# Optimization experiments

Hardware: AMD Instinct MI355X
Metric: run time of the kernel (lower is better)

## Reference

```python
import jax, jax.numpy as jnp
import numpy as np

# config
BSZ, L_, DM = 4, 2048, 1024
H, G, P, N, R = 16, 4, 64, 64, 2
RATIO = H // G            # 4
E, K = 64, 2              # kmoe experts / top_k
DPROJ = H * P * 2 + G * N * R * 2 + G * 3  # 3084


def rms(x, w, eps=1e-5):
    return x * jax.lax.rsqrt(jnp.mean(x * x, axis=-1, keepdims=True) + eps) * w


def kron_moe(x, router_w, A_e, B_e, scale, bias, d1, d2, o1, o2, k):
    # x: [..., d1*d2] -> [..., o1*o2]
    orig = x.shape
    xf = x.reshape(-1, d1 * d2)
    logits = xf @ router_w.T                       # [T, E]
    vals, idx = jax.lax.top_k(logits, k)           # [T, k]
    probs = jax.nn.softmax(vals, axis=-1)
    xs = xf.reshape(-1, d1, d2)
    # Y[t,k,o,p] = sum_ij A[t,k,o,i] x[t,i,j] B[t,k,p,j]
    Y = jnp.einsum('tkoi,tij,tkpj->tkop', A_e[idx], xs, B_e[idx])
    out = jnp.sum(Y * probs[:, :, None, None], axis=1).reshape(orig[:-1] + (o1 * o2,))
    return out * scale + bias


def setup_inputs() -> dict:
    key = jax.random.key(0)
    ks = jax.random.split(key, 12)
    r = lambda k, s, sc: jax.random.normal(k, s, jnp.float32) * sc
    return dict(
        u=jax.random.normal(ks[0], (BSZ, L_, DM), jnp.float32),
        in_proj_w=r(ks[1], (DPROJ, DM), 0.02),
        in_proj_b=jnp.zeros((DPROJ,), jnp.float32),
        xup_router=r(ks[2], (E, P), 0.02),
        xup_A=r(ks[3], (E, 8, 8), 0.1),
        xup_B=r(ks[4], (E, 16, 8), 0.1),
        xup_scale=jnp.ones((1,), jnp.float32),
        xup_bias=jnp.zeros((P * R,), jnp.float32),
        ydown_w=r(ks[5], (P, P * R), 0.02),
        oup_router=r(ks[6], (E, H * P), 0.02),
        oup_A=r(ks[7], (E, 32, 32), 0.05),
        oup_B=r(ks[8], (E, 32, 32), 0.05),
        oup_scale=jnp.ones((1,), jnp.float32),
        oup_bias=jnp.zeros((DM,), jnp.float32),
        theta_log=r(ks[9], (G, N // 2), 1.0),
        D=jnp.ones((H,), jnp.float32),
        normB_w=jnp.ones((N * R,), jnp.float32),
        normC_w=jnp.ones((N * R,), jnp.float32),
        bias_B=jnp.zeros((G, N, R), jnp.float32),
        bias_C=jnp.zeros((G, N, R), jnp.float32),
        pregate_w=jnp.ones((H * P,), jnp.float32),
    )


def reference(u, in_proj_w, in_proj_b, xup_router, xup_A, xup_B, xup_scale, xup_bias,
              ydown_w, oup_router, oup_A, oup_B, oup_scale, oup_bias,
              theta_log, D, normB_w, normC_w, bias_B, bias_C, pregate_w):
    B, L, _ = u.shape
    HP, GNR = H * P, G * N * R
    proj = u @ in_proj_w.T + in_proj_b
    splits = np.cumsum([HP, HP, GNR, GNR, G, G])
    z, x_p, Bp, Cp, dt, A_p, lam = jnp.split(proj, splits, axis=-1)
    dt = jax.nn.softplus(dt)                       # [B,L,G]
    A = -jnp.exp(A_p)                              # [B,L,G]
    theta = jnp.exp(theta_log)                     # [G,N/2]
    Bp = rms(Bp.reshape(B, L, G, N * R), normB_w).reshape(B, L, G, N, R) + bias_B
    Cp = rms(Cp.reshape(B, L, G, N * R), normC_w).reshape(B, L, G, N, R) + bias_C
    angles_g = jnp.cumsum(dt[..., None] * theta[None, None], axis=1)   # [B,L,G,N/2]
    rep = lambda v: jnp.repeat(v, RATIO, axis=2)   # group -> head broadcast
    angles = rep(angles_g)                         # [B,L,H,N/2]
    dt_h = rep(dt[..., None])                      # [B,L,H,1]
    A_h = rep(A[..., None])                        # [B,L,H,1]
    B_h, C_h = rep(Bp), rep(Cp)                    # [B,L,H,N,R]
    cos = jnp.cos(angles)[..., None]
    sin = jnp.sin(angles)[..., None]

    def rotate(v):
        re, im = v[..., 0::2, :], v[..., 1::2, :]
        return jnp.stack([re * cos - im * sin, re * sin + im * cos], axis=-2).reshape(v.shape)

    B_rot, C_rot = rotate(B_h), rotate(C_h)
    x = kron_moe(x_p.reshape(B, L, H, P), xup_router, xup_A, xup_B, xup_scale, xup_bias,
                 8, 8, 8, 16, K).reshape(B, L, H, P, R)
    alpha = jnp.exp(dt_h * A_h)[..., None]         # [B,L,H,1,1]

    mv = lambda v: jnp.moveaxis(v, 1, 0)           # time-major for scan

    def step(h, xs):
        Br, Cr, xt, at, dtt = xs
        in_sig = jnp.einsum('bhnr,bhpr->bhnp', Br, xt)
        h = h * at + dtt[..., None] * in_sig
        y_t = jnp.einsum('bhnp,bhnr->bhpr', h, Cr)
        return h, y_t

    h0 = jnp.zeros((B, H, N, P), u.dtype)
    _, ys = jax.lax.scan(step, h0, (mv(B_rot), mv(C_rot), mv(x), mv(alpha), mv(dt_h)))
    y = jnp.moveaxis(ys, 0, 1)                     # [B,L,H,P,R]
    y = (y.reshape(B, L, H, P * R) @ ydown_w.T).reshape(B, L, H * P)
    y = rms(y + x_p * jnp.repeat(D, P), pregate_w) * jax.nn.sigmoid(z)
    out = kron_moe(y, oup_router, oup_A, oup_B, oup_scale, oup_bias, 32, 32, 32, 32, K)
    return out
```

## Files before the change

kernel.cpp:

```cpp
#include <hip/hip_runtime.h>
#include <hip/hip_bf16.h>
#include <math.h>

namespace {
constexpr int kB = 4, kL = 2048, kDM = 1024;
constexpr int kH = 16, kG = 4;
constexpr int kDPROJ = 3084;
constexpr int COL_Z = 0, COL_XP = 1024, COL_B = 2048, COL_C = 2560, COL_DT = 3072, COL_A = 3076;
constexpr int kTOK = kB * kL;
constexpr int kNC = kL / 64;
constexpr int kNPAD = 3200;
constexpr float kLOG2E = 1.4426950408889634f;
}

typedef __attribute__((ext_vector_type(8))) __bf16 bf16x8;
typedef __attribute__((ext_vector_type(8))) unsigned short u16x8;
typedef __attribute__((ext_vector_type(4))) float f32x4;

#define GLDS16(gp, lp)                                                          \
  __builtin_amdgcn_global_load_lds(                                             \
      (const __attribute__((address_space(1))) void*)(gp),                      \
      (__attribute__((address_space(3))) void*)(lp), 16, 0, 0)

__device__ __forceinline__ unsigned short bf16_rne(float f) {
  unsigned u = __builtin_bit_cast(unsigned, f);
  unsigned r = u + 0x7fffu + ((u >> 16) & 1u);
  return (unsigned short)(r >> 16);
}
__device__ __forceinline__ void split2(float f, unsigned short& h, unsigned short& l) {
  unsigned short hh = bf16_rne(f);
  float hf = __builtin_bit_cast(float, (unsigned)hh << 16);
  h = hh;
  l = bf16_rne(f - hf);
}
__device__ __forceinline__ bf16x8 ldsb8(const unsigned short* p) {
  return __builtin_bit_cast(bf16x8, *(const u16x8*)p);
}

__global__ __launch_bounds__(256) void k_split_u(const float* __restrict__ X,
                                                 unsigned short* __restrict__ hi,
                                                 unsigned short* __restrict__ lo) {
  int i = blockIdx.x * 256 + threadIdx.x;
  float4 x = ((const float4*)X)[i];
  float xs[4] = {x.x, x.y, x.z, x.w};
  ushort4 hv, lv;
  unsigned short hq[4], lq[4];
#pragma unroll
  for (int q = 0; q < 4; ++q) split2(xs[q], hq[q], lq[q]);
  hv.x = hq[0]; hv.y = hq[1]; hv.z = hq[2]; hv.w = hq[3];
  lv.x = lq[0]; lv.y = lq[1]; lv.z = lq[2]; lv.w = lq[3];
  ((ushort4*)hi)[i] = hv;
  ((ushort4*)lo)[i] = lv;
}

__global__ __launch_bounds__(256) void k_split_w(const float* __restrict__ X,
                                                 unsigned short* __restrict__ hi,
                                                 unsigned short* __restrict__ lo) {
  int i = blockIdx.x * 256 + threadIdx.x;
  int row = i >> 8;
  float4 x = make_float4(0.f, 0.f, 0.f, 0.f);
  if (row < kDPROJ) x = ((const float4*)X)[i];
  float xs[4] = {x.x, x.y, x.z, x.w};
  ushort4 hv, lv;
  unsigned short hq[4], lq[4];
#pragma unroll
  for (int q = 0; q < 4; ++q) split2(xs[q], hq[q], lq[q]);
  hv.x = hq[0]; hv.y = hq[1]; hv.z = hq[2]; hv.w = hq[3];
  lv.x = lq[0]; lv.y = lq[1]; lv.z = lq[2]; lv.w = lq[3];
  ((ushort4*)hi)[i] = hv;
  ((ushort4*)lo)[i] = lv;
}

__global__ __launch_bounds__(256) void k_inproj_mfma(
    const unsigned short* __restrict__ Uhi, const unsigned short* __restrict__ Ulo,
    const unsigned short* __restrict__ Whi, const unsigned short* __restrict__ Wlo,
    const float* __restrict__ bias, float* __restrict__ proj) {
  __shared__ unsigned short lds_u[16384];
  const int tid = threadIdx.x;
  const int wave = tid >> 6, lane = tid & 63;
  const int wm = wave >> 1, wn = wave & 1;
  const int row0 = blockIdx.x * 128, col0 = blockIdx.y * 128;
  const int fr = lane & 15, kq = lane >> 4;

  f32x4 acc[4][4];
#pragma unroll
  for (int i = 0; i < 4; ++i)
#pragma unroll
    for (int j = 0; j < 4; ++j) acc[i][j] = (f32x4){0.f, 0.f, 0.f, 0.f};

  const int s0 = wave * 64 + lane;

  for (int k0 = 0; k0 < kDM; k0 += 32) {
#pragma unroll
    for (int q = 0; q < 2; ++q) {
      const int slot = q * 256 + s0;
      const int r = slot >> 2;
      const int ce = ((slot & 3) ^ ((r >> 1) & 3)) * 8;
      const size_t ao = (size_t)(row0 + r) * kDM + k0 + ce;
      const size_t bo = (size_t)(col0 + r) * kDM + k0 + ce;
      const int lb = (q * 256 + wave * 64) * 16;
      GLDS16(Uhi + ao, (char*)lds_u + lb);
      GLDS16(Ulo + ao, (char*)lds_u + 8192 + lb);
      GLDS16(Whi + bo, (char*)lds_u + 16384 + lb);
      GLDS16(Wlo + bo, (char*)lds_u + 24576 + lb);
    }
    __syncthreads();
    bf16x8 ahi[4], alo[4], bhi[4], blo[4];
#pragma unroll
    for (int mi = 0; mi < 4; ++mi) {
      int r = wm * 64 + mi * 16 + fr;
      int off = r * 32 + ((kq ^ ((r >> 1) & 3)) * 8);
      ahi[mi] = ldsb8(lds_u + off);
      alo[mi] = ldsb8(lds_u + 4096 + off);
    }
#pragma unroll
    for (int ni = 0; ni < 4; ++ni) {
      int r = wn * 64 + ni * 16 + fr;
      int off = r * 32 + ((kq ^ ((r >> 1) & 3)) * 8);
      bhi[ni] = ldsb8(lds_u + 8192 + off);
      blo[ni] = ldsb8(lds_u + 12288 + off);
    }
#pragma unroll
    for (int mi = 0; mi < 4; ++mi)
#pragma unroll
      for (int ni = 0; ni < 4; ++ni) {
        acc[mi][ni] = __builtin_amdgcn_mfma_f32_16x16x32_bf16(ahi[mi], bhi[ni], acc[mi][ni], 0, 0, 0);
        acc[mi][ni] = __builtin_amdgcn_mfma_f32_16x16x32_bf16(ahi[mi], blo[ni], acc[mi][ni], 0, 0, 0);
        acc[mi][ni] = __builtin_amdgcn_mfma_f32_16x16x32_bf16(alo[mi], bhi[ni], acc[mi][ni], 0, 0, 0);
      }
    __syncthreads();
  }

  const int orow = row0 + wm * 64, ocol = col0 + wn * 64;
#pragma unroll
  for (int mi = 0; mi < 4; ++mi)
#pragma unroll
    for (int ni = 0; ni < 4; ++ni) {
      int cg = ocol + ni * 16 + fr;
      if (cg < kDPROJ) {
        float bv = bias[cg];
#pragma unroll
        for (int r = 0; r < 4; ++r) {
          int rg = orow + mi * 16 + kq * 4 + r;
          proj[(size_t)rg * kDPROJ + cg] = acc[mi][ni][r] + bv;
        }
      }
    }
}

__global__ __launch_bounds__(256) void k_dtprep(const float* __restrict__ proj,
                                                float* __restrict__ dtg,
                                                float* __restrict__ cumalog,
                                                double* __restrict__ cumdt) {
  int bg = blockIdx.x;
  int b = bg / kG, g = bg % kG;
  int tid = threadIdx.x;
  __shared__ double s_dt[256], s_al[256];
  double loc_dt[8], loc_al[8];
  double sdt = 0.0, sal = 0.0;
#pragma unroll
  for (int q = 0; q < 8; ++q) {
    int t = tid * 8 + q;
    size_t i = (size_t)(b * kL + t) * kDPROJ;
    float rd = proj[i + COL_DT + g];
    float ra = proj[i + COL_A + g];
    float dt = rd > 20.f ? rd : log1pf(expf(rd));
    float al = -expf(ra) * dt;
    dtg[(size_t)(b * kL + t) * kG + g] = dt;
    sdt += (double)dt; loc_dt[q] = sdt;
    sal += (double)al; loc_al[q] = sal;
  }
  s_dt[tid] = sdt; s_al[tid] = sal;
  __syncthreads();
  for (int off = 1; off < 256; off <<= 1) {
    double a = 0.0, c = 0.0;
    if (tid >= off) { a = s_dt[tid - off]; c = s_al[tid - off]; }
    __syncthreads();
    s_dt[tid] += a; s_al[tid] += c;
    __syncthreads();
  }
  double base_dt = tid ? s_dt[tid - 1] : 0.0;
  double base_al = tid ? s_al[tid - 1] : 0.0;
#pragma unroll
  for (int q = 0; q < 8; ++q) {
    int t = tid * 8 + q;
    size_t idx = (size_t)(b * kL + t) * kG + g;
    cumdt[idx] = base_dt + loc_dt[q];
    cumalog[idx] = (float)(base_al + loc_al[q]);
  }
}

__global__ __launch_bounds__(256) void k_angles(const double* __restrict__ cumdt,
                                                const float* __restrict__ theta_log,
                                                float* __restrict__ cs_tab) {
  int idx = blockIdx.x * 256 + threadIdx.x;
  int tok = idx >> 7, gk = idx & 127, g = gk >> 5, k = gk & 31;
  double theta = exp((double)theta_log[g * 32 + k]);
  double ang = theta * cumdt[(size_t)tok * kG + g];
  const double twopi = 6.283185307179586476925286766559;
  double rem = ang - floor(ang / twopi) * twopi;
  cs_tab[(size_t)idx * 2] = cosf((float)rem);
  cs_tab[(size_t)idx * 2 + 1] = sinf((float)rem);
}

__global__ __launch_bounds__(256) void k_rotate(float* __restrict__ proj,
                                                const float* __restrict__ cs_tab,
                                                const float* __restrict__ normB_w,
                                                const float* __restrict__ normC_w,
                                                const float* __restrict__ bias_B,
                                                const float* __restrict__ bias_C) {
  int tok = blockIdx.x;
  int tid = threadIdx.x;
  __shared__ float buf[256];
  __shared__ float red[4];
  size_t rowoff = (size_t)tok * kDPROJ;
  int half = tid >> 7;
  int j = tid & 127;
  int wave = tid >> 6;
  for (int g = 0; g < kG; ++g) {
    int col = (half ? COL_C : COL_B) + g * 128 + j;
    float v = proj[rowoff + col];
    float ss = v * v;
    for (int o = 1; o < 64; o <<= 1) ss += __shfl_xor(ss, o);
    if ((tid & 63) == 0) red[wave] = ss;
    __syncthreads();
    float tot = red[half * 2] + red[half * 2 + 1];
    float scale = rsqrtf(tot / 128.f + 1e-5f);
    const float* nw = half ? normC_w : normB_w;
    const float* bb = half ? bias_C : bias_B;
    float nv = v * scale * nw[j] + bb[g * 128 + j];
    buf[tid] = nv;
    __syncthreads();
    float other = buf[tid ^ 2];
    int n = j >> 1, k = n >> 1;
    bool isRe = (n & 1) == 0;
    const float* cs = cs_tab + (((size_t)tok * kG + g) * 32 + k) * 2;
    float cc = cs[0], sn = cs[1];
    float out = isRe ? (nv * cc - other * sn) : (other * sn + nv * cc);
    proj[rowoff + col] = out;
    __syncthreads();
  }
}

__global__ __launch_bounds__(256) void k_xup(const float* __restrict__ proj,
                                             const float* __restrict__ router,
                                             const float* __restrict__ Ae,
                                             const float* __restrict__ Be,
                                             const float* __restrict__ scale_,
                                             const float* __restrict__ bias_,
                                             float* __restrict__ xmoe) {
  int wave = threadIdx.x >> 6, lane = threadIdx.x & 63;
  int unit = blockIdx.x * 4 + wave;
  int tok = unit >> 4, h = unit & 15;
  __shared__ float xs_all[4][64];
  __shared__ float Rs[64][65];
  for (int m = threadIdx.x; m < 64 * 64; m += 256) Rs[m >> 6][m & 63] = router[m];
  float xv = proj[(size_t)tok * kDPROJ + COL_XP + h * 64 + lane];
  xs_all[wave][lane] = xv;
  __syncthreads();
  const float* xs = xs_all[wave];
  double accd = 0.0;
#pragma unroll
  for (int d = 0; d < 64; ++d) accd += (double)Rs[lane][d] * (double)xs[d];
  float logit = (float)accd;
  float v1 = logit; int i1 = lane;
  for (int o = 1; o < 64; o <<= 1) {
    float vv = __shfl_xor(v1, o); int ii = __shfl_xor(i1, o);
    if (vv > v1 || (vv == v1 && ii < i1)) { v1 = vv; i1 = ii; }
  }
  float lm = (lane == i1) ? -INFINITY : logit;
  float v2 = lm; int i2 = lane;
  for (int o = 1; o < 64; o <<= 1) {
    float vv = __shfl_xor(v2, o); int ii = __shfl_xor(i2, o);
    if (vv > v2 || (vv == v2 && ii < i2)) { v2 = vv; i2 = ii; }
  }
  float e12 = expf(v2 - v1);
  float p1 = 1.f / (1.f + e12), p2 = e12 / (1.f + e12);
  float out0 = 0.f, out1 = 0.f;
#pragma unroll
  for (int kk = 0; kk < 2; ++kk) {
    int e = kk ? i2 : i1;
    float pw = kk ? p2 : p1;
    const float* A = Ae + (size_t)e * 64;
    const float* Bm = Be + (size_t)e * 128;
#pragma unroll
    for (int hlf = 0; hlf < 2; ++hlf) {
      int c = lane + hlf * 64;
      int o = c >> 4, p = c & 15;
      float y = 0.f;
#pragma unroll
      for (int i = 0; i < 8; ++i) {
        float t = 0.f;
#pragma unroll
        for (int jj = 0; jj < 8; ++jj) t += xs[i * 8 + jj] * Bm[p * 8 + jj];
        y += A[o * 8 + i] * t;
      }
      if (hlf) out1 += pw * y; else out0 += pw * y;
    }
  }
  float sc = scale_[0];
  size_t ob = (size_t)unit * 128;
  xmoe[ob + lane] = out0 * sc + bias_[lane];
  xmoe[ob + lane + 64] = out1 * sc + bias_[lane + 64];
}

__global__ __launch_bounds__(256) void k_passA(const float* __restrict__ proj,
                                               const float* __restrict__ xmoe,
                                               const float* __restrict__ dtg,
                                               const float* __restrict__ cumalog,
                                               float* __restrict__ hstate) {
  int bid = blockIdx.x;
  int c = bid & 31, h = (bid >> 5) & 15, b = bid >> 9, g = h >> 2;
  int tid = threadIdx.x;
  __shared__ float Bs[128][65];
  __shared__ float Xs[128][65];
  __shared__ float wv[64];
  int base = c * 64;
  size_t tok0 = (size_t)b * kL + base;
  if (tid < 64) {
    float ca_last = cumalog[(tok0 + 63) * kG + g];
    float ca_s = cumalog[(tok0 + tid) * kG + g];
    float dt = dtg[(tok0 + tid) * kG + g];
    wv[tid] = expf(ca_last - ca_s) * dt;
  }
  __syncthreads();
  for (int m = tid; m < 8192; m += 256) {
    int s = m >> 7, j = m & 127;
    float bval = proj[(tok0 + s) * kDPROJ + COL_B + g * 128 + j];
    Bs[s * 2 + (j & 1)][j >> 1] = bval * wv[s];
    float xval = xmoe[((tok0 + s) * kH + h) * (size_t)128 + j];
    Xs[s * 2 + (j & 1)][j >> 1] = xval;
  }
  __syncthreads();
  int tx = tid & 15, ty = tid >> 4;
  float acc[4][4];
#pragma unroll
  for (int i = 0; i < 4; ++i)
#pragma unroll
    for (int j = 0; j < 4; ++j) acc[i][j] = 0.f;
  for (int k = 0; k < 128; ++k) {
    float a[4], bv[4];
#pragma unroll
    for (int q = 0; q < 4; ++q) a[q] = Bs[k][ty * 4 + q];
#pragma unroll
    for (int q = 0; q < 4; ++q) bv[q] = Xs[k][tx * 4 + q];
#pragma unroll
    for (int i = 0; i < 4; ++i)
#pragma unroll
      for (int j = 0; j < 4; ++j) acc[i][j] += a[i] * bv[j];
  }
  float* out = hstate + (size_t)bid * 4096;
#pragma unroll
  for (int i = 0; i < 4; ++i)
#pragma unroll
    for (int j = 0; j < 4; ++j)
      out[(ty * 4 + i) * 64 + tx * 4 + j] = acc[i][j];
}

__global__ __launch_bounds__(256) void k_passB(float* __restrict__ hstate,
                                               const float* __restrict__ cumalog) {
  int bh = blockIdx.x;
  int b = bh >> 4, h = bh & 15, g = h >> 2;
  int tid = threadIdx.x;
  float hrun[16];
#pragma unroll
  for (int q = 0; q < 16; ++q) hrun[q] = 0.f;
  float* Hbase = hstate + (size_t)bh * 32 * 4096;
  for (int c = 0; c < 32; ++c) {
    float ca_last = cumalog[((size_t)b * kL + c * 64 + 63) * kG + g];
    float ca_prev = c ? cumalog[((size_t)b * kL + c * 64 - 1) * kG + g] : 0.f;
    float Dc = expf(ca_last - ca_prev);
    float* Hc = Hbase + (size_t)c * 4096;
#pragma unroll
    for (int q = 0; q < 16; ++q) {
      int idx = tid + q * 256;
      float local = Hc[idx];
      Hc[idx] = hrun[q];
      hrun[q] = Dc * hrun[q] + local;
    }
  }
}

namespace {
constexpr int SC = 72;
constexpr int SG = 136;
constexpr int SH = 72;
constexpr int SW = 66;
}
__global__ __launch_bounds__(1024) void k_passC(const float* __restrict__ proj,
                                                const float* __restrict__ xmoe,
                                                const float* __restrict__ dtg,
                                                const float* __restrict__ cumalog,
                                                const float* __restrict__ hstate,
                                                const float* __restrict__ ydown,
                                                float* __restrict__ outY) {
  __shared__ __align__(16) char smem[162560];
  unsigned short* sCh = (unsigned short*)smem;
  unsigned short* sCl = sCh + 128 * SC;
  unsigned short* sBh = (unsigned short*)(smem + 36864);
  unsigned short* sBl = sBh + 128 * SC;
  float*          sW  = (float*)(smem + 73728);
  unsigned short* sHh = (unsigned short*)(smem + 73728);
  unsigned short* sHl = sHh + 64 * SH;
  unsigned short* sGh = (unsigned short*)(smem + 92160);
  unsigned short* sGl = sGh + 128 * SG;
  float* sca  = (float*)(smem + 161792);
  float* sdts = sca + 64;
  float* selx = sdts + 64;
  unsigned short* sXh  = (unsigned short*)smem;
  unsigned short* sXl  = sXh + 64 * SG;
  unsigned short* sWdh = (unsigned short*)(smem + 36864);
  unsigned short* sWdl = sWdh + 64 * SG;
  unsigned short* sYh  = (unsigned short*)(smem + 92160);
  unsigned short* sYl  = sYh + 64 * SG;

  int bid = blockIdx.x;
  int c = bid & 31, h = (bid >> 5) & 15, b = bid >> 9, g = h >> 2;
  int tid = threadIdx.x;
  const int wave = tid >> 6, lane = tid & 63;
  const int fr = lane & 15, kq = lane >> 4;
  int base = c * 64;
  size_t tok0 = (size_t)b * kL + base;
  size_t projBase = tok0 * kDPROJ;

  if (tid < 64) {
    float ca_prev = base ? cumalog[(tok0 - 1) * kG + g] : 0.f;
    float ca_t = cumalog[(tok0 + tid) * kG + g];
    sca[tid] = ca_t;
    sdts[tid] = dtg[(tok0 + tid) * kG + g];
    selx[tid] = exp2f((ca_t - ca_prev) * kLOG2E);
  }
  for (int m = tid; m < 8192; m += 1024) {
    int s = m >> 7, j = m & 127;
    int row = s * 2 + (j & 1), col = j >> 1;
    unsigned short hh, ll;
    float cv = proj[projBase + (size_t)s * kDPROJ + COL_C + g * 128 + j];
    split2(cv, hh, ll);
    sCh[row * SC + col] = hh; sCl[row * SC + col] = ll;
    float bv = proj[projBase + (size_t)s * kDPROJ + COL_B + g * 128 + j];
    split2(bv, hh, ll);
    sBh[row * SC + col] = hh; sBl[row * SC + col] = ll;
  }
  __syncthreads();

  for (int m = tid; m < 4096; m += 1024) {
    int t = m >> 6, s = m & 63;
    float w = (s <= t) ? sdts[s] * exp2f((sca[t] - sca[s]) * kLOG2E) : 0.f;
    sW[t * SW + s] = w;
  }
  const int rowA0 = (wave & 7) * 16;
  const int colH = wave >> 3;
  f32x4 gacc[4];
#pragma unroll
  for (int j = 0; j < 4; ++j) gacc[j] = (f32x4){0.f, 0.f, 0.f, 0.f};
#pragma unroll
  for (int ks = 0; ks < 2; ++ks) {
    int kb = ks * 32 + kq * 8;
    int offA = (rowA0 + fr) * SC + kb;
    bf16x8 ah = ldsb8(sCh + offA);
    bf16x8 al = ldsb8(sCl + offA);
#pragma unroll
    for (int ni = 0; ni < 4; ++ni) {
      int off = (colH * 64 + ni * 16 + fr) * SC + kb;
      bf16x8 bh = ldsb8(sBh + off);
      bf16x8 bl = ldsb8(sBl + off);
      gacc[ni] = __builtin_amdgcn_mfma_f32_16x16x32_bf16(ah, bh, gacc[ni], 0, 0, 0);
      gacc[ni] = __builtin_amdgcn_mfma_f32_16x16x32_bf16(ah, bl, gacc[ni], 0, 0, 0);
      gacc[ni] = __builtin_amdgcn_mfma_f32_16x16x32_bf16(al, bh, gacc[ni], 0, 0, 0);
    }
  }
  __syncthreads();

#pragma unroll
  for (int ni = 0; ni < 4; ++ni) {
    int colg = colH * 64 + ni * 16 + fr;
    int s = colg >> 1;
#pragma unroll
    for (int r = 0; r < 4; ++r) {
      int rowg = rowA0 + kq * 4 + r;
      int t = rowg >> 1;
      float gm = gacc[ni][r] * sW[t * SW + s];
      unsigned short hh, ll;
      split2(gm, hh, ll);
      sGh[rowg * SG + colg] = hh;
      sGl[rowg * SG + colg] = ll;
    }
  }
  __syncthreads();

  for (int m = tid; m < 4096; m += 1024) {
    int n = m >> 6, p = m & 63;
    float v = hstate[(size_t)bid * 4096 + m];
    unsigned short hh, ll;
    split2(v, hh, ll);
    sHh[p * SH + n] = hh;
    sHl[p * SH + n] = ll;
  }
  __syncthreads();

  f32x4 yac[2];
#pragma unroll
  for (int j = 0; j < 2; ++j) yac[j] = (f32x4){0.f, 0.f, 0.f, 0.f};
#pragma unroll
  for (int ks = 0; ks < 2; ++ks) {
    int kb = ks * 32 + kq * 8;
    int offA = (rowA0 + fr) * SC + kb;
    bf16x8 ah = ldsb8(sCh + offA);
    bf16x8 al = ldsb8(sCl + offA);
#pragma unroll
    for (int ni = 0; ni < 2; ++ni) {
      int off = (colH * 32 + ni * 16 + fr) * SH + kb;
      bf16x8 bh = ldsb8(sHh + off);
      bf16x8 bl = ldsb8(sHl + off);
      yac[ni] = __builtin_amdgcn_mfma_f32_16x16x32_bf16(ah, bh, yac[ni], 0, 0, 0);
      yac[ni] = __builtin_amdgcn_mfma_f32_16x16x32_bf16(ah, bl, yac[ni], 0, 0, 0);
      yac[ni] = __builtin_amdgcn_mfma_f32_16x16x32_bf16(al, bh, yac[ni], 0, 0, 0);
    }
  }
#pragma unroll
  for (int r = 0; r < 4; ++r) {
    int t = (rowA0 + kq * 4 + r) >> 1;
    float e = selx[t];
#pragma unroll
    for (int ni = 0; ni < 2; ++ni) yac[ni][r] *= e;
  }
  __syncthreads();

  for (int m = tid; m < 8192; m += 1024) {
    int s = m >> 7, j = m & 127;
    float xv = xmoe[((tok0 + s) * kH + h) * (size_t)128 + j];
    int p = j >> 1, cc = s * 2 + (j & 1);
    unsigned short hh, ll;
    split2(xv, hh, ll);
    sXh[p * SG + cc] = hh; sXl[p * SG + cc] = ll;
    float wv = ydown[m];
    split2(wv, hh, ll);
    sWdh[(m >> 7) * SG + (m & 127)] = hh;
    sWdl[(m >> 7) * SG + (m & 127)] = ll;
  }
  __syncthreads();

#pragma unroll
  for (int ks = 0; ks < 4; ++ks) {
    int kb = ks * 32 + kq * 8;
    int offA = (rowA0 + fr) * SG + kb;
    bf16x8 ah = ldsb8(sGh + offA);
    bf16x8 al = ldsb8(sGl + offA);
#pragma unroll
    for (int ni = 0; ni < 2; ++ni) {
      int off = (colH * 32 + ni * 16 + fr) * SG + kb;
      bf16x8 bh = ldsb8(sXh + off);
      bf16x8 bl = ldsb8(sXl + off);
      yac[ni] = __builtin_amdgcn_mfma_f32_16x16x32_bf16(ah, bh, yac[ni], 0, 0, 0);
      yac[ni] = __builtin_amdgcn_mfma_f32_16x16x32_bf16(ah, bl, yac[ni], 0, 0, 0);
      yac[ni] = __builtin_amdgcn_mfma_f32_16x16x32_bf16(al, bh, yac[ni], 0, 0, 0);
    }
  }
  __syncthreads();

#pragma unroll
  for (int ni = 0; ni < 2; ++ni)
#pragma unroll
    for (int r = 0; r < 4; ++r) {
      int rowg = rowA0 + kq * 4 + r;
      int t = rowg >> 1, rr = rowg & 1;
      int p = colH * 32 + ni * 16 + fr;
      unsigned short hh, ll;
      split2(yac[ni][r], hh, ll);
      sYh[t * SG + p * 2 + rr] = hh;
      sYl[t * SG + p * 2 + rr] = ll;
    }
  __syncthreads();

  f32x4 zac = (f32x4){0.f, 0.f, 0.f, 0.f};
  const int zr0 = (wave & 3) * 16, zc0 = (wave >> 2) * 16;
#pragma unroll
  for (int ks = 0; ks < 4; ++ks) {
    int kb = ks * 32 + kq * 8;
    int offA = (zr0 + fr) * SG + kb;
    bf16x8 ah = ldsb8(sYh + offA);
    bf16x8 al = ldsb8(sYl + offA);
    int offB = (zc0 + fr) * SG + kb;
    bf16x8 bh = ldsb8(sWdh + offB);
    bf16x8 bl = ldsb8(sWdl + offB);
    zac = __builtin_amdgcn_mfma_f32_16x16x32_bf16(ah, bh, zac, 0, 0, 0);
    zac = __builtin_amdgcn_mfma_f32_16x16x32_bf16(ah, bl, zac, 0, 0, 0);
    zac = __builtin_amdgcn_mfma_f32_16x16x32_bf16(al, bh, zac, 0, 0, 0);
  }
#pragma unroll
  for (int r = 0; r < 4; ++r) {
    int t = zr0 + kq * 4 + r;
    int o = zc0 + fr;
    outY[(tok0 + t) * (size_t)1024 + h * 64 + o] = zac[r];
  }
}

__global__ __launch_bounds__(256) void k_gate(float* __restrict__ y,
                                              const float* __restrict__ proj,
                                              const float* __restrict__ Dv,
                                              const float* __restrict__ pregate_w) {
  int tok = blockIdx.x;
  int tid = threadIdx.x;
  size_t yoff = (size_t)tok * 1024;
  size_t poff = (size_t)tok * kDPROJ;
  __shared__ float red[4];
  float vals[4];
  float ss = 0.f;
#pragma unroll
  for (int q = 0; q < 4; ++q) {
    int j = tid + q * 256;
    float v = y[yoff + j] + proj[poff + COL_XP + j] * Dv[j >> 6];
    vals[q] = v;
    ss += v * v;
  }
  for (int o = 1; o < 64; o <<= 1) ss += __shfl_xor(ss, o);
  if ((tid & 63) == 0) red[tid >> 6] = ss;
  __syncthreads();
  float tot = red[0] + red[1] + red[2] + red[3];
  float scale = rsqrtf(tot / 1024.f + 1e-5f);
#pragma unroll
  for (int q = 0; q < 4; ++q) {
    int j = tid + q * 256;
    float z = proj[poff + COL_Z + j];
    float sig = 1.f / (1.f + expf(-z));
    y[yoff + j] = vals[q] * scale * pregate_w[j] * sig;
  }
}

__global__ __launch_bounds__(256) void k_logits(const float* __restrict__ y,
                                                const float* __restrict__ router,
                                                float* __restrict__ logits) {
  __shared__ float Yt[16][65];
  __shared__ float Rt[64][65];
  int tid = threadIdx.x;
  int tok0 = blockIdx.x * 16;
  int t = tid & 15;
  int e0 = (tid >> 4) * 4;
  double acc[4] = {0.0, 0.0, 0.0, 0.0};
  for (int kc = 0; kc < 1024; kc += 64) {
    for (int m = tid; m < 1024; m += 256) {
      int tt = m >> 6, c = m & 63;
      Yt[tt][c] = y[(size_t)(tok0 + tt) * 1024 + kc + c];
    }
    for (int m = tid; m < 4096; m += 256) {
      int ee = m >> 6, c = m & 63;
      Rt[ee][c] = router[(size_t)ee * 1024 + kc + c];
    }
    __syncthreads();
    for (int c = 0; c < 64; ++c) {
      float yv = Yt[t][c];
#pragma unroll
      for (int i = 0; i < 4; ++i)
        acc[i] += (double)Rt[e0 + i][c] * (double)yv;
    }
    __syncthreads();
  }
#pragma unroll
  for (int i = 0; i < 4; ++i)
    logits[(size_t)(tok0 + t) * 64 + e0 + i] = (float)acc[i];
}

__global__ __launch_bounds__(256) void k_oup(float* __restrict__ y,
                                             const float* __restrict__ logits,
                                             const float* __restrict__ Ae,
                                             const float* __restrict__ Be,
                                             const float* __restrict__ scale_,
                                             const float* __restrict__ bias_) {
  int tok = blockIdx.x;
  int tid = threadIdx.x;
  __shared__ float xs[1024];
  __shared__ float Ts[32][33];
  __shared__ float lg[64];
  size_t yoff = (size_t)tok * 1024;
  for (int m = tid; m < 1024; m += 256) xs[m] = y[yoff + m];
  if (tid < 64) lg[tid] = logits[(size_t)tok * 64 + tid];
  __syncthreads();
  float v1 = -INFINITY; int i1 = -1;
  for (int e = 0; e < 64; ++e) { float v = lg[e]; if (v > v1) { v1 = v; i1 = e; } }
  float v2 = -INFINITY; int i2 = -1;
  for (int e = 0; e < 64; ++e) { if (e == i1) continue; float v = lg[e]; if (v > v2) { v2 = v; i2 = e; } }
  float e12 = expf(v2 - v1);
  float p1 = 1.f / (1.f + e12), p2 = e12 / (1.f + e12);
  float out[4] = {0.f, 0.f, 0.f, 0.f};
  for (int kk = 0; kk < 2; ++kk) {
    int e = kk ? i2 : i1;
    float pw = kk ? p2 : p1;
    const float* A = Ae + (size_t)e * 1024;
    const float* Bm = Be + (size_t)e * 1024;
    __syncthreads();
    for (int m = tid; m < 1024; m += 256) {
      int i = m >> 5, p = m & 31;
      float t = 0.f;
#pragma unroll
      for (int j = 0; j < 32; ++j) t += xs[i * 32 + j] * Bm[p * 32 + j];
      Ts[i][p] = t;
    }
    __syncthreads();
#pragma unroll
    for (int q = 0; q < 4; ++q) {
      int cc = tid + q * 256;
      int o = cc >> 5, p = cc & 31;
      float a2 = 0.f;
#pragma unroll
      for (int i = 0; i < 32; ++i) a2 += A[o * 32 + i] * Ts[i][p];
      out[q] += pw * a2;
    }
  }
  float sc = scale_[0];
#pragma unroll
  for (int q = 0; q < 4; ++q) {
    int cc = tid + q * 256;
    y[yoff + cc] = out[q] * sc + bias_[cc];
  }
}

extern "C" void kernel_launch(void* const* d_in, const int* in_sizes, int n_in,
                              void* d_out, int out_size, void* d_ws, size_t ws_size,
                              hipStream_t stream) {
  const float* u          = (const float*)d_in[0];
  const float* in_proj_w  = (const float*)d_in[1];
  const float* in_proj_b  = (const float*)d_in[2];
  const float* xup_router = (const float*)d_in[3];
  const float* xup_A      = (const float*)d_in[4];
  const float* xup_B      = (const float*)d_in[5];
  const float* xup_scale  = (const float*)d_in[6];
  const float* xup_bias   = (const float*)d_in[7];
  const float* ydown_w    = (const float*)d_in[8];
  const float* oup_router = (const float*)d_in[9];
  const float* oup_A      = (const float*)d_in[10];
  const float* oup_B      = (const float*)d_in[11];
  const float* oup_scale  = (const float*)d_in[12];
  const float* oup_bias   = (const float*)d_in[13];
  const float* theta_log  = (const float*)d_in[14];
  const float* Dv         = (const float*)d_in[15];
  const float* normB_w    = (const float*)d_in[16];
  const float* normC_w    = (const float*)d_in[17];
  const float* bias_B     = (const float*)d_in[18];
  const float* bias_C     = (const float*)d_in[19];
  const float* pregate_w  = (const float*)d_in[20];

  char* ws = (char*)d_ws;
  float* proj = (float*)ws;      ws += (size_t)kTOK * kDPROJ * 4;
  float* dtg = (float*)ws;       ws += (size_t)kTOK * kG * 4;
  float* cumalog = (float*)ws;   ws += (size_t)kTOK * kG * 4;
  double* cumdt = (double*)ws;   ws += (size_t)kTOK * kG * 8;
  float* cs_tab = (float*)ws;    ws += (size_t)kTOK * kG * 32 * 2 * 4;
  float* xmoe = (float*)ws;      ws += (size_t)kTOK * kH * 128 * 4;
  float* hstate = (float*)ws;    ws += (size_t)kB * kH * kNC * 4096 * 4;
  float* outY = (float*)d_out;

  float* logits = cs_tab;

  unsigned short* Uhi = (unsigned short*)xmoe;
  unsigned short* Ulo = Uhi + (size_t)kTOK * kDM;
  unsigned short* Whi = Ulo + (size_t)kTOK * kDM;
  unsigned short* Wlo = Whi + (size_t)kNPAD * kDM;

  k_split_u<<<dim3(kTOK * kDM / 4 / 256), dim3(256), 0, stream>>>(u, Uhi, Ulo);
  k_split_w<<<dim3(kNPAD * kDM / 4 / 256), dim3(256), 0, stream>>>(in_proj_w, Whi, Wlo);
  k_inproj_mfma<<<dim3(kTOK / 128, kNPAD / 128), dim3(256), 0, stream>>>(Uhi, Ulo, Whi, Wlo, in_proj_b, proj);
  k_dtprep<<<dim3(kB * kG), dim3(256), 0, stream>>>(proj, dtg, cumalog, cumdt);
  k_angles<<<dim3(kTOK * 128 / 256), dim3(256), 0, stream>>>(cumdt, theta_log, cs_tab);
  k_rotate<<<dim3(kTOK), dim3(256), 0, stream>>>(proj, cs_tab, normB_w, normC_w, bias_B, bias_C);
  k_xup<<<dim3(kTOK * kH / 4), dim3(256), 0, stream>>>(proj, xup_router, xup_A, xup_B, xup_scale, xup_bias, xmoe);
  k_passA<<<dim3(kB * kH * kNC), dim3(256), 0, stream>>>(proj, xmoe, dtg, cumalog, hstate);
  k_passB<<<dim3(kB * kH), dim3(256), 0, stream>>>(hstate, cumalog);
  k_passC<<<dim3(kB * kH * kNC), dim3(1024), 0, stream>>>(proj, xmoe, dtg, cumalog, hstate, ydown_w, outY);
  k_gate<<<dim3(kTOK), dim3(256), 0, stream>>>(outY, proj, Dv, pregate_w);
  k_logits<<<dim3(kTOK / 16), dim3(256), 0, stream>>>(outY, oup_router, logits);
  k_oup<<<dim3(kTOK), dim3(256), 0, stream>>>(outY, logits, oup_A, oup_B, oup_scale, oup_bias);
}
```

Measured before the change: 856.5 us.

## Swizzle inproj grid, MFMA chunk-state pass, parallelize passB and rotate

Several independent changes. The in-projection GEMM moves to a 1D grid with a block-index swizzle, so that consecutive blocks share column tiles for better cache reuse. The chunk-state kernel (passA) now uses split-bf16 MFMA instead of a scalar FP32 outer-product loop. passB is split 8 ways across the state elements to get more parallelism, and k_rotate processes all four groups in one 1024-thread block instead of looping. The xup router dot product also gets four independent double accumulators, which shortens the dependency chain at the cost of a slightly different summation order.

```diff
diff --git a/kernel.cpp b/kernel.cpp
--- a/kernel.cpp
+++ b/kernel.cpp
@@ -79,7 +79,9 @@
   const int tid = threadIdx.x;
   const int wave = tid >> 6, lane = tid & 63;
   const int wm = wave >> 1, wn = wave & 1;
-  const int row0 = blockIdx.x * 128, col0 = blockIdx.y * 128;
+  const int orig = blockIdx.x;
+  const int swz = (orig & 7) * 200 + (orig >> 3);
+  const int row0 = (swz & 63) * 128, col0 = (swz >> 6) * 128;
   const int fr = lane & 15, kq = lane >> 4;
 
   f32x4 acc[4][4];
@@ -203,43 +205,42 @@
   cs_tab[(size_t)idx * 2 + 1] = sinf((float)rem);
 }
 
-__global__ __launch_bounds__(256) void k_rotate(float* __restrict__ proj,
-                                                const float* __restrict__ cs_tab,
-                                                const float* __restrict__ normB_w,
-                                                const float* __restrict__ normC_w,
-                                                const float* __restrict__ bias_B,
-                                                const float* __restrict__ bias_C) {
+__global__ __launch_bounds__(1024) void k_rotate(float* __restrict__ proj,
+                                                 const float* __restrict__ cs_tab,
+                                                 const float* __restrict__ normB_w,
+                                                 const float* __restrict__ normC_w,
+                                                 const float* __restrict__ bias_B,
+                                                 const float* __restrict__ bias_C) {
   int tok = blockIdx.x;
   int tid = threadIdx.x;
-  __shared__ float buf[256];
-  __shared__ float red[4];
+  __shared__ float buf[1024];
+  __shared__ float red[16];
   size_t rowoff = (size_t)tok * kDPROJ;
-  int half = tid >> 7;
+  int g = tid >> 8;
+  int half = (tid >> 7) & 1;
   int j = tid & 127;
   int wave = tid >> 6;
-  for (int g = 0; g < kG; ++g) {
-    int col = (half ? COL_C : COL_B) + g * 128 + j;
-    float v = proj[rowoff + col];
-    float ss = v * v;
-    for (int o = 1; o < 64; o <<= 1) ss += __shfl_xor(ss, o);
-    if ((tid & 63) == 0) red[wave] = ss;
-    __syncthreads();
-    float tot = red[half * 2] + red[half * 2 + 1];
-    float scale = rsqrtf(tot / 128.f + 1e-5f);
-    const float* nw = half ? normC_w : normB_w;
-    const float* bb = half ? bias_C : bias_B;
-    float nv = v * scale * nw[j] + bb[g * 128 + j];
-    buf[tid] = nv;
-    __syncthreads();
-    float other = buf[tid ^ 2];
-    int n = j >> 1, k = n >> 1;
-    bool isRe = (n & 1) == 0;
-    const float* cs = cs_tab + (((size_t)tok * kG + g) * 32 + k) * 2;
-    float cc = cs[0], sn = cs[1];
-    float out = isRe ? (nv * cc - other * sn) : (other * sn + nv * cc);
-    proj[rowoff + col] = out;
-    __syncthreads();
-  }
+  int col = (half ? COL_C : COL_B) + g * 128 + j;
+  float v = proj[rowoff + col];
+  float ss = v * v;
+  for (int o = 1; o < 64; o <<= 1) ss += __shfl_xor(ss, o);
+  if ((tid & 63) == 0) red[wave] = ss;
+  __syncthreads();
+  float tot = red[wave] + red[wave ^ 1];
+  float scale = rsqrtf(tot / 128.f + 1e-5f);
+  const float* nw = half ? normC_w : normB_w;
+  const float* bb = half ? bias_C : bias_B;
+  float nv = v * scale * nw[j] + bb[g * 128 + j];
+  buf[tid] = nv;
+  __syncthreads();
+  float other = buf[tid ^ 2];
+  int n = j >> 1;
+  int k = n >> 1;
+  bool isRe = (n & 1) == 0;
+  const float* cs = cs_tab + (((size_t)tok * kG + g) * 32 + k) * 2;
+  float cc = cs[0], sn = cs[1];
+  float out = isRe ? (nv * cc - other * sn) : (other * sn + nv * cc);
+  proj[rowoff + col] = out;
 }
 
 __global__ __launch_bounds__(256) void k_xup(const float* __restrict__ proj,
@@ -259,10 +260,15 @@
   xs_all[wave][lane] = xv;
   __syncthreads();
   const float* xs = xs_all[wave];
-  double accd = 0.0;
-#pragma unroll
-  for (int d = 0; d < 64; ++d) accd += (double)Rs[lane][d] * (double)xs[d];
-  float logit = (float)accd;
+  double a0 = 0.0, a1 = 0.0, a2 = 0.0, a3 = 0.0;
+#pragma unroll
+  for (int d = 0; d < 64; d += 4) {
+    a0 += (double)Rs[lane][d + 0] * (double)xs[d + 0];
+    a1 += (double)Rs[lane][d + 1] * (double)xs[d + 1];
+    a2 += (double)Rs[lane][d + 2] * (double)xs[d + 2];
+    a3 += (double)Rs[lane][d + 3] * (double)xs[d + 3];
+  }
+  float logit = (float)((a0 + a1) + (a2 + a3));
   float v1 = logit; int i1 = lane;
   for (int o = 1; o < 64; o <<= 1) {
     float vv = __shfl_xor(v1, o); int ii = __shfl_xor(i1, o);
@@ -304,17 +310,22 @@
   xmoe[ob + lane + 64] = out1 * sc + bias_[lane + 64];
 }
 
+namespace { constexpr int SK = 136; }
 __global__ __launch_bounds__(256) void k_passA(const float* __restrict__ proj,
                                                const float* __restrict__ xmoe,
                                                const float* __restrict__ dtg,
                                                const float* __restrict__ cumalog,
                                                float* __restrict__ hstate) {
+  __shared__ unsigned short sBh[64 * SK];
+  __shared__ unsigned short sBl[64 * SK];
+  __shared__ unsigned short sXh[64 * SK];
+  __shared__ unsigned short sXl[64 * SK];
+  __shared__ float wv[64];
   int bid = blockIdx.x;
   int c = bid & 31, h = (bid >> 5) & 15, b = bid >> 9, g = h >> 2;
   int tid = threadIdx.x;
-  __shared__ float Bs[128][65];
-  __shared__ float Xs[128][65];
-  __shared__ float wv[64];
+  const int wave = tid >> 6, lane = tid & 63;
+  const int fr = lane & 15, kq = lane >> 4;
   int base = c * 64;
   size_t tok0 = (size_t)b * kL + base;
   if (tid < 64) {
@@ -326,53 +337,62 @@
   __syncthreads();
   for (int m = tid; m < 8192; m += 256) {
     int s = m >> 7, j = m & 127;
-    float bval = proj[(tok0 + s) * kDPROJ + COL_B + g * 128 + j];
-    Bs[s * 2 + (j & 1)][j >> 1] = bval * wv[s];
+    int k = s * 2 + (j & 1), n = j >> 1;
+    unsigned short hh, ll;
+    float bval = proj[(tok0 + s) * kDPROJ + COL_B + g * 128 + j] * wv[s];
+    split2(bval, hh, ll);
+    sBh[n * SK + k] = hh; sBl[n * SK + k] = ll;
     float xval = xmoe[((tok0 + s) * kH + h) * (size_t)128 + j];
-    Xs[s * 2 + (j & 1)][j >> 1] = xval;
-  }
-  __syncthreads();
-  int tx = tid & 15, ty = tid >> 4;
-  float acc[4][4];
-#pragma unroll
-  for (int i = 0; i < 4; ++i)
-#pragma unroll
-    for (int j = 0; j < 4; ++j) acc[i][j] = 0.f;
-  for (int k = 0; k < 128; ++k) {
-    float a[4], bv[4];
-#pragma unroll
-    for (int q = 0; q < 4; ++q) a[q] = Bs[k][ty * 4 + q];
-#pragma unroll
-    for (int q = 0; q < 4; ++q) bv[q] = Xs[k][tx * 4 + q];
-#pragma unroll
-    for (int i = 0; i < 4; ++i)
-#pragma unroll
-      for (int j = 0; j < 4; ++j) acc[i][j] += a[i] * bv[j];
+    split2(xval, hh, ll);
+    sXh[n * SK + k] = hh; sXl[n * SK + k] = ll;
+  }
+  __syncthreads();
+  const int n0 = wave * 16;
+  f32x4 acc[4];
+#pragma unroll
+  for (int j = 0; j < 4; ++j) acc[j] = (f32x4){0.f, 0.f, 0.f, 0.f};
+#pragma unroll
+  for (int ks = 0; ks < 4; ++ks) {
+    int kb = ks * 32 + kq * 8;
+    int offA = (n0 + fr) * SK + kb;
+    bf16x8 ah = ldsb8(sBh + offA);
+    bf16x8 al = ldsb8(sBl + offA);
+#pragma unroll
+    for (int ni = 0; ni < 4; ++ni) {
+      int offB = (ni * 16 + fr) * SK + kb;
+      bf16x8 bh = ldsb8(sXh + offB);
+      bf16x8 bl = ldsb8(sXl + offB);
+      acc[ni] = __builtin_amdgcn_mfma_f32_16x16x32_bf16(ah, bh, acc[ni], 0, 0, 0);
+      acc[ni] = __builtin_amdgcn_mfma_f32_16x16x32_bf16(ah, bl, acc[ni], 0, 0, 0);
+      acc[ni] = __builtin_amdgcn_mfma_f32_16x16x32_bf16(al, bh, acc[ni], 0, 0, 0);
+    }
   }
   float* out = hstate + (size_t)bid * 4096;
 #pragma unroll
-  for (int i = 0; i < 4; ++i)
-#pragma unroll
-    for (int j = 0; j < 4; ++j)
-      out[(ty * 4 + i) * 64 + tx * 4 + j] = acc[i][j];
+  for (int ni = 0; ni < 4; ++ni)
+#pragma unroll
+    for (int r = 0; r < 4; ++r) {
+      int n = n0 + kq * 4 + r;
+      int p = ni * 16 + fr;
+      out[n * 64 + p] = acc[ni][r];
+    }
 }
 
 __global__ __launch_bounds__(256) void k_passB(float* __restrict__ hstate,
                                                const float* __restrict__ cumalog) {
-  int bh = blockIdx.x;
-  int b = bh >> 4, h = bh & 15, g = h >> 2;
+  int bid = blockIdx.x;
+  int q8 = bid & 7, bh = bid >> 3;
+  int b = bh >> 4, g = (bh & 15) >> 2;
   int tid = threadIdx.x;
-  float hrun[16];
-#pragma unroll
-  for (int q = 0; q < 16; ++q) hrun[q] = 0.f;
-  float* Hbase = hstate + (size_t)bh * 32 * 4096;
+  float hrun[2] = {0.f, 0.f};
+  float* Hbase = hstate + (size_t)bh * 32 * 4096 + q8 * 512;
   for (int c = 0; c < 32; ++c) {
     float ca_last = cumalog[((size_t)b * kL + c * 64 + 63) * kG + g];
     float ca_prev = c ? cumalog[((size_t)b * kL + c * 64 - 1) * kG + g] : 0.f;
     float Dc = expf(ca_last - ca_prev);
     float* Hc = Hbase + (size_t)c * 4096;
 #pragma unroll
-    for (int q = 0; q < 16; ++q) {
+    for (int q = 0; q < 2; ++q) {
       int idx = tid + q * 256;
       float local = Hc[idx];
       Hc[idx] = hrun[q];
@@ -533,8 +553,8 @@
     unsigned short hh, ll;
     split2(xv, hh, ll);
     sXh[p * SG + cc] = hh; sXl[p * SG + cc] = ll;
-    float wv = ydown[m];
-    split2(wv, hh, ll);
+    float wv2 = ydown[m];
+    split2(wv2, hh, ll);
     sWdh[(m >> 7) * SG + (m & 127)] = hh;
     sWdl[(m >> 7) * SG + (m & 127)] = ll;
   }
@@ -758,13 +778,13 @@
 
   k_split_u<<<dim3(kTOK * kDM / 4 / 256), dim3(256), 0, stream>>>(u, Uhi, Ulo);
   k_split_w<<<dim3(kNPAD * kDM / 4 / 256), dim3(256), 0, stream>>>(in_proj_w, Whi, Wlo);
-  k_inproj_mfma<<<dim3(kTOK / 128, kNPAD / 128), dim3(256), 0, stream>>>(Uhi, Ulo, Whi, Wlo, in_proj_b, proj);
+  k_inproj_mfma<<<dim3((kTOK / 128) * (kNPAD / 128)), dim3(256), 0, stream>>>(Uhi, Ulo, Whi, Wlo, in_proj_b, proj);
   k_dtprep<<<dim3(kB * kG), dim3(256), 0, stream>>>(proj, dtg, cumalog, cumdt);
   k_angles<<<dim3(kTOK * 128 / 256), dim3(256), 0, stream>>>(cumdt, theta_log, cs_tab);
-  k_rotate<<<dim3(kTOK), dim3(256), 0, stream>>>(proj, cs_tab, normB_w, normC_w, bias_B, bias_C);
+  k_rotate<<<dim3(kTOK), dim3(1024), 0, stream>>>(proj, cs_tab, normB_w, normC_w, bias_B, bias_C);
   k_xup<<<dim3(kTOK * kH / 4), dim3(256), 0, stream>>>(proj, xup_router, xup_A, xup_B, xup_scale, xup_bias, xmoe);
   k_passA<<<dim3(kB * kH * kNC), dim3(256), 0, stream>>>(proj, xmoe, dtg, cumalog, hstate);
-  k_passB<<<dim3(kB * kH), dim3(256), 0, stream>>>(hstate, cumalog);
+  k_passB<<<dim3(kB * kH * 8), dim3(256), 0, stream>>>(hstate, cumalog);
   k_passC<<<dim3(kB * kH * kNC), dim3(1024), 0, stream>>>(proj, xmoe, dtg, cumalog, hstate, ydown_w, outY);
   k_gate<<<dim3(kTOK), dim3(256), 0, stream>>>(outY, proj, Dv, pregate_w);
   k_logits<<<dim3(kTOK / 16), dim3(256), 0, stream>>>(outY, oup_router, logits);
```

After: 860.3 us. No clear change (+0.4%).
